# Optimization experiments

Measured on AMD Instinct MI355X. Metric: run time of the kernel, lower is better.

The kernel has to match this reference:

```python
import jax, jax.numpy as jnp
import numpy as np

FEATURES = 512
SPLIT_TT = 2
DK = FEATURES // SPLIT_TT           # 256: key width = features // split_tt
NUM_TAPE = 2048                     # ac_config.num_tape_tokens
THRESHOLD = 4.0                     # ac_config.dynamic_tape_length.act_epsilon
TOPK = int(NUM_TAPE // THRESHOLD)   # 512
TOKENS_PER_STEP = 16                # num_token_per_step
BATCH = 64


def setup_inputs() -> dict:
    key = jax.random.key(0)
    kq, kt = jax.random.split(key)
    return {
        "query": jax.random.normal(kq, (BATCH, DK), jnp.float32),
        "halting_prob": jnp.zeros((BATCH,), jnp.float32),
        "remainders": jnp.zeros((BATCH,), jnp.float32),
        "n_updates": jnp.zeros((BATCH,), jnp.float32),
        "score_mask": jnp.zeros((BATCH, NUM_TAPE), jnp.float32),
        "tape_tokens": jax.random.normal(kt, (BATCH, NUM_TAPE, FEATURES), jnp.float32),
    }


def reference(query, halting_prob, remainders, n_updates, score_mask, tape_tokens):
    # One ACT step (take_a_step / act_step) with bank_type='input',
    # act_loss_type='entropy', complex_query=True.
    still_running = (halting_prob < THRESHOLD).astype(jnp.float32)   # [B]

    # keys are the first DK features of the per-example tape bank
    keys = tape_tokens[:, :, :DK]                                    # [B, N, DK]
    scores = jnp.einsum('bd,bnd->bn', query, keys)                   # [B, N]

    # mask already-selected tokens, then top-k
    topk_idx = jax.lax.top_k(scores - score_mask * 1e9, TOPK)[1]     # [B, K] int32

    # NOTE: faithful to original: jnp.take without axis => FLAT gather into
    # scores.ravel(); indices in [0, N) all address row 0 of scores.
    weights = jnp.take(scores, topk_idx)                             # [B, K]
    weights = jax.nn.softmax(weights / (query.shape[-1] ** 0.5), axis=-1)

    entropy = 1.0 - jnp.sum(weights ** 2, axis=-1)                   # [B]
    sum_weights = jnp.sum(weights[:, :TOKENS_PER_STEP], axis=-1)     # [B]

    new_halted = (halting_prob + sum_weights >= THRESHOLD).astype(jnp.float32) * still_running
    still_running = still_running - new_halted
    remainders = remainders + (new_halted + still_running) * entropy
    halting_prob = halting_prob + sum_weights * still_running
    halting_prob = halting_prob + new_halted * (THRESHOLD - halting_prob)
    n_updates = n_updates + still_running + new_halted

    # gather selected tape tokens per example, softmax-weighted merge
    token_sel = jnp.take_along_axis(tape_tokens, topk_idx[..., None], axis=1)  # [B, K, F]
    token_sel = jnp.sum(token_sel * weights[..., None], axis=-2, keepdims=True)  # [B, 1, F]

    # scatter-accumulate selection mask
    score_mask = score_mask + jnp.sum(jax.nn.one_hot(topk_idx, NUM_TAPE), axis=1)  # [B, N]

    # complex_query update
    token_sel_keys = token_sel[:, :, :DK]                            # [B, 1, DK]
    query = (query + jnp.mean(token_sel_keys, axis=1)) / 2.0         # [B, DK]

    return (query, halting_prob, remainders, n_updates, score_mask, token_sel)
```

## Files before the change

### kernel.cpp

```cpp
#include <hip/hip_runtime.h>
#include <math.h>

#define BATCH 64
#define DK 256
#define FEATURES 512
#define NUM_TAPE 2048
#define TOPK 512
#define TOP16 16
#define THRESH 4.0f
#define KCHUNKS 4
#define KPER (TOPK / KCHUNKS)
#define CAP 640

#define OFF_Q 0
#define OFF_HP (BATCH * DK)
#define OFF_REM (OFF_HP + BATCH)
#define OFF_NUP (OFF_REM + BATCH)
#define OFF_MASK (OFF_NUP + BATCH)
#define OFF_TSEL (OFF_MASK + BATCH * NUM_TAPE)

#define WS_SCORES 0
#define WS_TOPK 131072
#define WS_WEIGHTS 163840
#define WS_PART 196608

__device__ __forceinline__ unsigned f2key(float f) {
    unsigned u = __float_as_uint(f);
    return (u & 0x80000000u) ? ~u : (u | 0x80000000u);
}

#define RADIX_FIND(KREM)                                              \
    {                                                                 \
        int v = 0, hcnt = 0;                                          \
        if (tid < 256) {                                              \
            hcnt = hist[tid];                                         \
            v = hcnt;                                                 \
            _Pragma("unroll") for (int off = 1; off < 64; off <<= 1) {\
                const int t = __shfl_down(v, off);                    \
                if (lane + off < 64) v += t;                          \
            }                                                         \
            if (lane == 0) chunkTot[wv] = v;                          \
        }                                                             \
        __syncthreads();                                              \
        if (tid < 256) {                                              \
            _Pragma("unroll") for (int w2 = 0; w2 < 4; ++w2)          \
                if (w2 > wv) v += chunkTot[w2];                       \
            if (v >= (KREM) && (v - hcnt) < (KREM)) {                 \
                sh_digit = tid;                                       \
                sh_hi = v - hcnt;                                     \
            }                                                         \
        }                                                             \
        __syncthreads();                                              \
    }

__global__ __launch_bounds__(256) void k_scores(const float* __restrict__ q,
                                                const float* __restrict__ tape,
                                                float* __restrict__ scores) {
    const int b = blockIdx.y;
    const int wave = threadIdx.x >> 6;
    const int lane = threadIdx.x & 63;
    const float4 qf = reinterpret_cast<const float4*>(q + b * DK)[lane];
    const int base = blockIdx.x * 32;
#pragma unroll
    for (int t = 0; t < 8; ++t) {
        const int tok = base + wave + 4 * t;
        const float4 tf =
            reinterpret_cast<const float4*>(tape + ((size_t)b * NUM_TAPE + tok) * FEATURES)[lane];
        float s = qf.x * tf.x + qf.y * tf.y + qf.z * tf.z + qf.w * tf.w;
#pragma unroll
        for (int off = 32; off; off >>= 1) s += __shfl_xor(s, off);
        if (lane == 0) scores[b * NUM_TAPE + tok] = s;
    }
}

__global__ __launch_bounds__(512) void k_topk(const float* __restrict__ scores,
                                              const float* __restrict__ mask_in,
                                              const float* __restrict__ hp_in,
                                              const float* __restrict__ rem_in,
                                              const float* __restrict__ nup_in,
                                              int* __restrict__ topk_ws,
                                              float* __restrict__ weights_ws,
                                              float* __restrict__ out) {
    const int b = blockIdx.x;
    const int tid = threadIdx.x;
    const int lane = tid & 63;
    const int wv = tid >> 6;

    __shared__ int hist[256];
    __shared__ int chunkTot[4];
    __shared__ int sh_digit, sh_hi;
    __shared__ unsigned ckey[CAP];
    __shared__ int cidx[CAP];
    __shared__ int csel[CAP];
    __shared__ int cand_n;
    __shared__ float redf[3][8];
    __shared__ int wtot[8];

    const float4 sc = reinterpret_cast<const float4*>(scores + (size_t)b * NUM_TAPE)[tid];
    const float4 mk = reinterpret_cast<const float4*>(mask_in + (size_t)b * NUM_TAPE)[tid];
    const float4 s0 = reinterpret_cast<const float4*>(scores)[tid];
    unsigned key[4];
    key[0] = f2key(sc.x - mk.x * 1e9f);
    key[1] = f2key(sc.y - mk.y * 1e9f);
    key[2] = f2key(sc.z - mk.z * 1e9f);
    key[3] = f2key(sc.w - mk.w * 1e9f);
    const float s0v[4] = {s0.x * 0.0625f, s0.y * 0.0625f, s0.z * 0.0625f, s0.w * 0.0625f};

    if (tid < 256) hist[tid] = 0;
    __syncthreads();
#pragma unroll
    for (int j = 0; j < 4; ++j) atomicAdd(&hist[key[j] >> 24], 1);
    __syncthreads();
    RADIX_FIND(TOPK);
    const unsigned B1 = (unsigned)sh_digit;
    const int aboveA = sh_hi;
    __syncthreads();

    if (tid < 256) hist[tid] = 0;
    __syncthreads();
#pragma unroll
    for (int j = 0; j < 4; ++j)
        if ((key[j] >> 24) == B1) atomicAdd(&hist[(key[j] >> 16) & 0xFF], 1);
    __syncthreads();
    RADIX_FIND(TOPK - aboveA);
    const unsigned P16 = (B1 << 8) | (unsigned)sh_digit;
    const int krem512 = (TOPK - aboveA) - sh_hi;
    __syncthreads();

    if (tid == 0) cand_n = 0;
    __syncthreads();
    int cpos[4];
#pragma unroll
    for (int j = 0; j < 4; ++j) {
        cpos[j] = -1;
        if ((key[j] >> 16) == P16) {
            const int p = atomicAdd(&cand_n, 1);
            if (p < CAP) {
                ckey[p] = key[j];
                cidx[p] = 4 * tid + j;
            }
            cpos[j] = p;
        }
    }
    __syncthreads();
    int cn = cand_n < CAP ? cand_n : CAP;
    for (int t = tid; t < cn; t += 512) {
        const unsigned k = ckey[t];
        const int i = cidx[t];
        int r = 0;
        for (int u = 0; u < cn; ++u) {
            const unsigned ko = ckey[u];
            r += (ko > k) || (ko == k && cidx[u] < i);
        }
        csel[t] = (r < krem512);
    }
    __syncthreads();
    bool sel[4];
#pragma unroll
    for (int j = 0; j < 4; ++j)
        sel[j] = ((key[j] >> 16) > P16) ||
                 (cpos[j] >= 0 && cpos[j] < CAP && csel[cpos[j]]);
    __syncthreads();

    if (tid < 256) hist[tid] = 0;
    __syncthreads();
#pragma unroll
    for (int j = 0; j < 4; ++j)
        if (sel[j]) atomicAdd(&hist[key[j] >> 24], 1);
    __syncthreads();
    RADIX_FIND(TOP16);
    const unsigned C1 = (unsigned)sh_digit;
    const int aboveC = sh_hi;
    __syncthreads();

    if (tid < 256) hist[tid] = 0;
    __syncthreads();
#pragma unroll
    for (int j = 0; j < 4; ++j)
        if (sel[j] && (key[j] >> 24) == C1) atomicAdd(&hist[(key[j] >> 16) & 0xFF], 1);
    __syncthreads();
    RADIX_FIND(TOP16 - aboveC);
    const unsigned P16_2 = (C1 << 8) | (unsigned)sh_digit;
    const int krem16 = (TOP16 - aboveC) - sh_hi;
    __syncthreads();

    if (tid == 0) cand_n = 0;
    __syncthreads();
    int c2pos[4];
#pragma unroll
    for (int j = 0; j < 4; ++j) {
        c2pos[j] = -1;
        if (sel[j] && (key[j] >> 16) == P16_2) {
            const int p = atomicAdd(&cand_n, 1);
            if (p < CAP) {
                ckey[p] = key[j];
                cidx[p] = 4 * tid + j;
            }
            c2pos[j] = p;
        }
    }
    __syncthreads();
    cn = cand_n < CAP ? cand_n : CAP;
    for (int t = tid; t < cn; t += 512) {
        const unsigned k = ckey[t];
        const int i = cidx[t];
        int r = 0;
        for (int u = 0; u < cn; ++u) {
            const unsigned ko = ckey[u];
            r += (ko > k) || (ko == k && cidx[u] < i);
        }
        csel[t] = (r < krem16);
    }
    __syncthreads();
    bool in16[4];
#pragma unroll
    for (int j = 0; j < 4; ++j)
        in16[j] = sel[j] && (((key[j] >> 16) > P16_2) ||
                             (c2pos[j] >= 0 && c2pos[j] < CAP && csel[c2pos[j]]));

    float ev[4];
    float se = 0.f, se2 = 0.f, s16l = 0.f;
#pragma unroll
    for (int j = 0; j < 4; ++j) {
        ev[j] = sel[j] ? expf(s0v[j]) : 0.f;
        se += ev[j];
        se2 += ev[j] * ev[j];
        if (in16[j]) s16l += ev[j];
    }
#pragma unroll
    for (int off = 32; off; off >>= 1) {
        se += __shfl_xor(se, off);
        se2 += __shfl_xor(se2, off);
        s16l += __shfl_xor(s16l, off);
    }
    if (lane == 0) {
        redf[0][wv] = se;
        redf[1][wv] = se2;
        redf[2][wv] = s16l;
    }
    __syncthreads();
    float S = 0.f, S2 = 0.f, S16 = 0.f;
#pragma unroll
    for (int w2 = 0; w2 < 8; ++w2) {
        S += redf[0][w2];
        S2 += redf[1][w2];
        S16 += redf[2][w2];
    }
    const float inv = 1.0f / S;
    const float sumsq = S2 * inv * inv;
    const float s16 = S16 * inv;

    float w[4];
#pragma unroll
    for (int j = 0; j < 4; ++j) w[j] = ev[j] * inv;

    {
        const int cnt = (sel[0] ? 1 : 0) + (sel[1] ? 1 : 0) + (sel[2] ? 1 : 0) + (sel[3] ? 1 : 0);
        int pre = cnt;
#pragma unroll
        for (int off = 1; off < 64; off <<= 1) {
            const int t = __shfl_up(pre, off);
            if (lane >= off) pre += t;
        }
        if (lane == 63) wtot[wv] = pre;
        __syncthreads();
        int base = 0;
        for (int w2 = 0; w2 < wv; ++w2) base += wtot[w2];
        int p = base + pre - cnt;
#pragma unroll
        for (int j = 0; j < 4; ++j) {
            if (sel[j]) {
                topk_ws[b * TOPK + p] = 4 * tid + j;
                weights_ws[b * TOPK + p] = w[j];
                ++p;
            }
        }
    }

    if (tid == 0) {
        const float hp = hp_in[b], rem = rem_in[b], nup = nup_in[b];
        const float entropy = 1.0f - sumsq;
        const float still = (hp < THRESH) ? 1.f : 0.f;
        const float nh = ((hp + s16) >= THRESH ? 1.f : 0.f) * still;
        const float st2 = still - nh;
        out[OFF_REM + b] = rem + (nh + st2) * entropy;
        float hp1 = hp + s16 * st2;
        hp1 = hp1 + nh * (THRESH - hp1);
        out[OFF_HP + b] = hp1;
        out[OFF_NUP + b] = nup + st2 + nh;
    }
    float4 om;
    om.x = mk.x + (sel[0] ? 1.f : 0.f);
    om.y = mk.y + (sel[1] ? 1.f : 0.f);
    om.z = mk.z + (sel[2] ? 1.f : 0.f);
    om.w = mk.w + (sel[3] ? 1.f : 0.f);
    reinterpret_cast<float4*>(out + OFF_MASK + (size_t)b * NUM_TAPE)[tid] = om;
}

__global__ __launch_bounds__(512) void k_gather(const float* __restrict__ tape,
                                                const int* __restrict__ topk_ws,
                                                const float* __restrict__ weights_ws,
                                                float* __restrict__ partials) {
    const int b = blockIdx.y;
    const int kc = blockIdx.x;
    const int rs = threadIdx.x >> 7;
    const int f4 = threadIdx.x & 127;
    __shared__ float wsh[KPER];
    __shared__ int ish[KPER];
    __shared__ float4 shacc[512];
    if (threadIdx.x < KPER) {
        wsh[threadIdx.x] = weights_ws[b * TOPK + kc * KPER + threadIdx.x];
        ish[threadIdx.x] = topk_ws[b * TOPK + kc * KPER + threadIdx.x];
    }
    __syncthreads();
    float4 acc = {0.f, 0.f, 0.f, 0.f};
#pragma unroll 4
    for (int k = rs; k < KPER; k += 4) {
        const float w = wsh[k];
        const float4 t =
            reinterpret_cast<const float4*>(tape + ((size_t)b * NUM_TAPE + ish[k]) * FEATURES)[f4];
        acc.x = fmaf(w, t.x, acc.x);
        acc.y = fmaf(w, t.y, acc.y);
        acc.z = fmaf(w, t.z, acc.z);
        acc.w = fmaf(w, t.w, acc.w);
    }
    shacc[threadIdx.x] = acc;
    __syncthreads();
    if (threadIdx.x < 128) {
        const float4 a0 = shacc[f4];
        const float4 a1 = shacc[128 + f4];
        const float4 a2 = shacc[256 + f4];
        const float4 a3 = shacc[384 + f4];
        float4 r;
        r.x = (a0.x + a1.x) + (a2.x + a3.x);
        r.y = (a0.y + a1.y) + (a2.y + a3.y);
        r.z = (a0.z + a1.z) + (a2.z + a3.z);
        r.w = (a0.w + a1.w) + (a2.w + a3.w);
        reinterpret_cast<float4*>(partials + ((size_t)b * KCHUNKS + kc) * FEATURES)[f4] = r;
    }
}

__global__ __launch_bounds__(128) void k_finish(const float* __restrict__ q,
                                                const float* __restrict__ partials,
                                                float* __restrict__ out) {
    const int b = blockIdx.x;
    const int f4 = threadIdx.x;
    const float4* pp = reinterpret_cast<const float4*>(partials + (size_t)b * KCHUNKS * FEATURES);
    const float4 a0 = pp[0 * 128 + f4];
    const float4 a1 = pp[1 * 128 + f4];
    const float4 a2 = pp[2 * 128 + f4];
    const float4 a3 = pp[3 * 128 + f4];
    float4 s;
    s.x = (a0.x + a1.x) + (a2.x + a3.x);
    s.y = (a0.y + a1.y) + (a2.y + a3.y);
    s.z = (a0.z + a1.z) + (a2.z + a3.z);
    s.w = (a0.w + a1.w) + (a2.w + a3.w);
    reinterpret_cast<float4*>(out + OFF_TSEL + (size_t)b * FEATURES)[f4] = s;
    if (f4 < 64) {
        const float4 qv = reinterpret_cast<const float4*>(q + (size_t)b * DK)[f4];
        float4 nq;
        nq.x = (qv.x + s.x) * 0.5f;
        nq.y = (qv.y + s.y) * 0.5f;
        nq.z = (qv.z + s.z) * 0.5f;
        nq.w = (qv.w + s.w) * 0.5f;
        reinterpret_cast<float4*>(out + OFF_Q + (size_t)b * DK)[f4] = nq;
    }
}

extern "C" void kernel_launch(void* const* d_in, const int* in_sizes, int n_in,
                              void* d_out, int out_size, void* d_ws, size_t ws_size,
                              hipStream_t stream) {
    const float* q = (const float*)d_in[0];
    const float* hp = (const float*)d_in[1];
    const float* rem = (const float*)d_in[2];
    const float* nup = (const float*)d_in[3];
    const float* mask = (const float*)d_in[4];
    const float* tape = (const float*)d_in[5];
    float* out = (float*)d_out;
    float* ws = (float*)d_ws;

    float* scores = ws + WS_SCORES;
    int* topk = (int*)(ws + WS_TOPK);
    float* weights = ws + WS_WEIGHTS;
    float* partials = ws + WS_PART;

    k_scores<<<dim3(NUM_TAPE / 32, BATCH), 256, 0, stream>>>(q, tape, scores);
    k_topk<<<BATCH, 512, 0, stream>>>(scores, mask, hp, rem, nup, topk, weights, out);
    k_gather<<<dim3(KCHUNKS, BATCH), 512, 0, stream>>>(tape, topk, weights, partials);
    k_finish<<<BATCH, 128, 0, stream>>>(q, partials, out);
}
```

Measured before the change: 48.05 us.

## Fuse top-k selection into gather kernel, recomputing selection per chunk block

Merges the top-k selection kernel and the weighted gather kernel into one launch. Each of the four chunk blocks per batch row redoes the full radix top-k and softmax, then keeps only its slice of indices and weights in shared memory. This removes a kernel launch and the workspace round trip for indices and weights. Histogram clearing is folded into the radix-find macro, which drops several barriers. The cost is four times the selection work per row and higher shared memory use per block.

Result: faster. 45.69 us (-4.9%).

```diff
diff --git a/kernel.cpp b/kernel.cpp
--- a/kernel.cpp
+++ b/kernel.cpp
@@ -20,9 +20,7 @@
 #define OFF_TSEL (OFF_MASK + BATCH * NUM_TAPE)
 
 #define WS_SCORES 0
-#define WS_TOPK 131072
-#define WS_WEIGHTS 163840
-#define WS_PART 196608
+#define WS_PART 131072
 
 __device__ __forceinline__ unsigned f2key(float f) {
     unsigned u = __float_as_uint(f);
@@ -34,6 +32,7 @@
         int v = 0, hcnt = 0;                                          \
         if (tid < 256) {                                              \
             hcnt = hist[tid];                                         \
+            hist[tid] = 0;                                            \
             v = hcnt;                                                 \
             _Pragma("unroll") for (int off = 1; off < 64; off <<= 1) {\
                 const int t = __shfl_down(v, off);                    \
@@ -73,15 +72,13 @@
     }
 }
 
-__global__ __launch_bounds__(512) void k_topk(const float* __restrict__ scores,
-                                              const float* __restrict__ mask_in,
-                                              const float* __restrict__ hp_in,
-                                              const float* __restrict__ rem_in,
-                                              const float* __restrict__ nup_in,
-                                              int* __restrict__ topk_ws,
-                                              float* __restrict__ weights_ws,
-                                              float* __restrict__ out) {
-    const int b = blockIdx.x;
+__global__ __launch_bounds__(512) void k_select_gather(
+    const float* __restrict__ scores, const float* __restrict__ mask_in,
+    const float* __restrict__ hp_in, const float* __restrict__ rem_in,
+    const float* __restrict__ nup_in, const float* __restrict__ tape,
+    float* __restrict__ partials, float* __restrict__ out) {
+    const int b = blockIdx.y;
+    const int kc = blockIdx.x;
     const int tid = threadIdx.x;
     const int lane = tid & 63;
     const int wv = tid >> 6;
@@ -95,6 +92,9 @@
     __shared__ int cand_n;
     __shared__ float redf[3][8];
     __shared__ int wtot[8];
+    __shared__ float gl_w[KPER];
+    __shared__ int gl_idx[KPER];
+    __shared__ float4 shacc[512];
 
     const float4 sc = reinterpret_cast<const float4*>(scores + (size_t)b * NUM_TAPE)[tid];
     const float4 mk = reinterpret_cast<const float4*>(mask_in + (size_t)b * NUM_TAPE)[tid];
@@ -114,10 +114,6 @@
     RADIX_FIND(TOPK);
     const unsigned B1 = (unsigned)sh_digit;
     const int aboveA = sh_hi;
-    __syncthreads();
-
-    if (tid < 256) hist[tid] = 0;
-    __syncthreads();
 #pragma unroll
     for (int j = 0; j < 4; ++j)
         if ((key[j] >> 24) == B1) atomicAdd(&hist[(key[j] >> 16) & 0xFF], 1);
@@ -125,7 +121,6 @@
     RADIX_FIND(TOPK - aboveA);
     const unsigned P16 = (B1 << 8) | (unsigned)sh_digit;
     const int krem512 = (TOPK - aboveA) - sh_hi;
-    __syncthreads();
 
     if (tid == 0) cand_n = 0;
     __syncthreads();
@@ -162,8 +157,6 @@
                  (cpos[j] >= 0 && cpos[j] < CAP && csel[cpos[j]]);
     __syncthreads();
 
-    if (tid < 256) hist[tid] = 0;
-    __syncthreads();
 #pragma unroll
     for (int j = 0; j < 4; ++j)
         if (sel[j]) atomicAdd(&hist[key[j] >> 24], 1);
@@ -171,10 +164,6 @@
     RADIX_FIND(TOP16);
     const unsigned C1 = (unsigned)sh_digit;
     const int aboveC = sh_hi;
-    __syncthreads();
-
-    if (tid < 256) hist[tid] = 0;
-    __syncthreads();
 #pragma unroll
     for (int j = 0; j < 4; ++j)
         if (sel[j] && (key[j] >> 24) == C1) atomicAdd(&hist[(key[j] >> 16) & 0xFF], 1);
@@ -182,7 +171,6 @@
     RADIX_FIND(TOP16 - aboveC);
     const unsigned P16_2 = (C1 << 8) | (unsigned)sh_digit;
     const int krem16 = (TOP16 - aboveC) - sh_hi;
-    __syncthreads();
 
     if (tid == 0) cand_n = 0;
     __syncthreads();
@@ -267,66 +255,57 @@
         int base = 0;
         for (int w2 = 0; w2 < wv; ++w2) base += wtot[w2];
         int p = base + pre - cnt;
+        const int lo = kc * KPER, hi = lo + KPER;
 #pragma unroll
         for (int j = 0; j < 4; ++j) {
             if (sel[j]) {
-                topk_ws[b * TOPK + p] = 4 * tid + j;
-                weights_ws[b * TOPK + p] = w[j];
+                if (p >= lo && p < hi) {
+                    gl_idx[p - lo] = 4 * tid + j;
+                    gl_w[p - lo] = w[j];
+                }
                 ++p;
             }
         }
     }
 
-    if (tid == 0) {
-        const float hp = hp_in[b], rem = rem_in[b], nup = nup_in[b];
-        const float entropy = 1.0f - sumsq;
-        const float still = (hp < THRESH) ? 1.f : 0.f;
-        const float nh = ((hp + s16) >= THRESH ? 1.f : 0.f) * still;
-        const float st2 = still - nh;
-        out[OFF_REM + b] = rem + (nh + st2) * entropy;
-        float hp1 = hp + s16 * st2;
-        hp1 = hp1 + nh * (THRESH - hp1);
-        out[OFF_HP + b] = hp1;
-        out[OFF_NUP + b] = nup + st2 + nh;
-    }
-    float4 om;
-    om.x = mk.x + (sel[0] ? 1.f : 0.f);
-    om.y = mk.y + (sel[1] ? 1.f : 0.f);
-    om.z = mk.z + (sel[2] ? 1.f : 0.f);
-    om.w = mk.w + (sel[3] ? 1.f : 0.f);
-    reinterpret_cast<float4*>(out + OFF_MASK + (size_t)b * NUM_TAPE)[tid] = om;
-}
-
-__global__ __launch_bounds__(512) void k_gather(const float* __restrict__ tape,
-                                                const int* __restrict__ topk_ws,
-                                                const float* __restrict__ weights_ws,
-                                                float* __restrict__ partials) {
-    const int b = blockIdx.y;
-    const int kc = blockIdx.x;
-    const int rs = threadIdx.x >> 7;
-    const int f4 = threadIdx.x & 127;
-    __shared__ float wsh[KPER];
-    __shared__ int ish[KPER];
-    __shared__ float4 shacc[512];
-    if (threadIdx.x < KPER) {
-        wsh[threadIdx.x] = weights_ws[b * TOPK + kc * KPER + threadIdx.x];
-        ish[threadIdx.x] = topk_ws[b * TOPK + kc * KPER + threadIdx.x];
-    }
-    __syncthreads();
+    if (kc == 0) {
+        if (tid == 0) {
+            const float hp = hp_in[b], rem = rem_in[b], nup = nup_in[b];
+            const float entropy = 1.0f - sumsq;
+            const float still = (hp < THRESH) ? 1.f : 0.f;
+            const float nh = ((hp + s16) >= THRESH ? 1.f : 0.f) * still;
+            const float st2 = still - nh;
+            out[OFF_REM + b] = rem + (nh + st2) * entropy;
+            float hp1 = hp + s16 * st2;
+            hp1 = hp1 + nh * (THRESH - hp1);
+            out[OFF_HP + b] = hp1;
+            out[OFF_NUP + b] = nup + st2 + nh;
+        }
+        float4 om;
+        om.x = mk.x + (sel[0] ? 1.f : 0.f);
+        om.y = mk.y + (sel[1] ? 1.f : 0.f);
+        om.z = mk.z + (sel[2] ? 1.f : 0.f);
+        om.w = mk.w + (sel[3] ? 1.f : 0.f);
+        reinterpret_cast<float4*>(out + OFF_MASK + (size_t)b * NUM_TAPE)[tid] = om;
+    }
+    __syncthreads();
+
+    const int rs = tid >> 7;
+    const int f4 = tid & 127;
     float4 acc = {0.f, 0.f, 0.f, 0.f};
 #pragma unroll 4
     for (int k = rs; k < KPER; k += 4) {
-        const float w = wsh[k];
+        const float ww = gl_w[k];
         const float4 t =
-            reinterpret_cast<const float4*>(tape + ((size_t)b * NUM_TAPE + ish[k]) * FEATURES)[f4];
-        acc.x = fmaf(w, t.x, acc.x);
-        acc.y = fmaf(w, t.y, acc.y);
-        acc.z = fmaf(w, t.z, acc.z);
-        acc.w = fmaf(w, t.w, acc.w);
-    }
-    shacc[threadIdx.x] = acc;
-    __syncthreads();
-    if (threadIdx.x < 128) {
+            reinterpret_cast<const float4*>(tape + ((size_t)b * NUM_TAPE + gl_idx[k]) * FEATURES)[f4];
+        acc.x = fmaf(ww, t.x, acc.x);
+        acc.y = fmaf(ww, t.y, acc.y);
+        acc.z = fmaf(ww, t.z, acc.z);
+        acc.w = fmaf(ww, t.w, acc.w);
+    }
+    shacc[tid] = acc;
+    __syncthreads();
+    if (tid < 128) {
         const float4 a0 = shacc[f4];
         const float4 a1 = shacc[128 + f4];
         const float4 a2 = shacc[256 + f4];
@@ -380,12 +359,10 @@
     float* ws = (float*)d_ws;
 
     float* scores = ws + WS_SCORES;
-    int* topk = (int*)(ws + WS_TOPK);
-    float* weights = ws + WS_WEIGHTS;
     float* partials = ws + WS_PART;
 
     k_scores<<<dim3(NUM_TAPE / 32, BATCH), 256, 0, stream>>>(q, tape, scores);
-    k_topk<<<BATCH, 512, 0, stream>>>(scores, mask, hp, rem, nup, topk, weights, out);
-    k_gather<<<dim3(KCHUNKS, BATCH), 512, 0, stream>>>(tape, topk, weights, partials);
+    k_select_gather<<<dim3(KCHUNKS, BATCH), 512, 0, stream>>>(
+        scores, mask, hp, rem, nup, tape, partials, out);
     k_finish<<<BATCH, 128, 0, stream>>>(q, partials, out);
 }
```
